# Kernel tuning notes

Hardware: AMD Instinct MI355X
Metric: run time of the kernel (lower is better)

The kernel has to match this reference:

```python
import jax, jax.numpy as jnp
import numpy as np

P = 8
PARENT = {0: -1, 1: 0, 2: 0, 3: 1, 4: 1, 5: 2, 6: 2, 7: 3}

def _topo_order(parent):
    order = [k for k in range(len(parent)) if parent[k] == -1]
    frontier = list(order)
    while frontier:
        cur = frontier.pop(0)
        for k in range(len(parent)):
            if parent[k] == cur:
                order.append(k)
                frontier.append(k)
    return order

ORDER = _topo_order(PARENT)

def so3_exponential_map(log_rot, eps=1e-4):
    # log_rot: [M,3]; pytorch3d-style Rodrigues with clamped squared norm
    nrms = jnp.sum(log_rot * log_rot, axis=-1)
    theta = jnp.sqrt(jnp.clip(nrms, eps))
    fac1 = jnp.sin(theta) / theta
    fac2 = (1.0 - jnp.cos(theta)) / (theta * theta)
    x, y, z = log_rot[:, 0], log_rot[:, 1], log_rot[:, 2]
    zero = jnp.zeros_like(x)
    K = jnp.stack([zero, -z, y, z, zero, -x, -y, x, zero], axis=-1).reshape(-1, 3, 3)
    I = jnp.eye(3, dtype=log_rot.dtype)
    return fac1[:, None, None] * K + fac2[:, None, None] * (K @ K) + I

def _normalize(v, axis=-1, eps=1e-12):
    return v / jnp.maximum(jnp.linalg.norm(v, axis=axis, keepdims=True), eps)

def setup_inputs():
    key = jax.random.key(0)
    ks = jax.random.split(key, 8)
    N, F, K, Pn = 32, 512, 64000, P
    s = 1.0 / np.sqrt(F)  # keep MLP activations sane
    x = jax.random.normal(ks[0], (N, F), jnp.float32)
    W1 = jax.random.normal(ks[1], (F, F), jnp.float32) * s
    b1 = jnp.zeros((F,), jnp.float32)
    W2 = jax.random.normal(ks[2], (F, F), jnp.float32) * s
    b2 = jnp.zeros((F,), jnp.float32)
    W3 = jax.random.normal(ks[3], (F, Pn * 5), jnp.float32) * s
    b3 = jnp.zeros((Pn * 5,), jnp.float32)
    verts = jax.random.normal(ks[4], (K, 3), jnp.float32)
    rot_center = jax.random.normal(ks[5], (Pn, 3), jnp.float32)
    alpha = jax.random.uniform(ks[6], (K, Pn), jnp.float32)
    alpha = alpha / jnp.sum(alpha, axis=-1, keepdims=True)  # LBS-style weights
    axis = jnp.tile(jnp.array([[1.0, 0.0, 0.0]], jnp.float32), (Pn, 1))
    return {"x": x, "W1": W1, "b1": b1, "W2": W2, "b2": b2, "W3": W3, "b3": b3,
            "verts": verts, "rot_center": rot_center, "alpha": alpha, "axis": axis}

def reference(x, W1, b1, W2, b2, W3, b3, verts, rot_center, alpha, axis):
    N = x.shape[0]
    lrelu = lambda h: jax.nn.leaky_relu(h, 0.01)
    h = lrelu(x @ W1 + b1)
    h = lrelu(h @ W2 + b2)
    vec = (h @ W3 + b3).reshape(N, P, 5)  # num_rots+num_trans = 5
    vec_rot = _normalize(vec[..., :3])    # vec[..., 0:num_rots+1]
    angle = jnp.arctan2(vec_rot[..., 1], vec_rot[..., 0])  # [N,P]
    axis_n = _normalize(axis)
    log_rot = angle[..., None] * axis_n[None]  # [N,P,3]
    R = so3_exponential_map(log_rot.reshape(-1, 3)).reshape(N, P, 3, 3)
    # t is forced to zero in the original forward (if True: t = zeros)
    t_part = rot_center[None] - jnp.einsum('npij,pj->npi', R, rot_center)  # [N,P,3]
    Rg = [None] * P
    tg = [None] * P
    for k in ORDER:  # tiny fixed tree (8 nodes), sequential chain composition
        p = PARENT[k]
        if p == -1:
            Rg[k] = R[:, k]
            tg[k] = t_part[:, k]
        else:
            Rg[k] = jnp.einsum('nij,njk->nik', Rg[p], R[:, k])
            tg[k] = jnp.einsum('nij,nj->ni', Rg[p], t_part[:, k]) + tg[p]
    Rg = jnp.stack(Rg, axis=1)  # [N,P,3,3]
    tg = jnp.stack(tg, axis=1)  # [N,P,3]
    # per-part transform applied to every vertex: [N,K,P,3]
    nsv = jnp.einsum('npij,kj->nkpi', Rg, verts) + tg[:, None]
    arti_verts = jnp.einsum('kp,nkpi->nki', alpha, nsv)  # [N,K,3]
    t_net = jnp.zeros((N, P, 3), x.dtype)
    return (arti_verts, t_net)
```

## Files before the change

### kernel.cpp

```cpp
#include <hip/hip_runtime.h>
#include <math.h>

#define FDIM 512
#define NBATCH 32
#define NPART 8
#define KVERT 64000

__global__ __launch_bounds__(256) void layer_k(const float* __restrict__ in,
                                               const float* __restrict__ W,
                                               const float* __restrict__ bias,
                                               float* __restrict__ out) {
  const int jt = blockIdx.x;
  const int n  = blockIdx.y;
  const int jj = threadIdx.x & 63;
  const int fq = threadIdx.x >> 6;
  const int j  = jt * 64 + jj;
  const float* xr = in + n * FDIM + fq * 128;
  const float* wp = W + (fq * 128) * FDIM + j;
  float acc0 = 0.f, acc1 = 0.f;
#pragma unroll
  for (int i = 0; i < 32; ++i) {
    const float4 xv = *(const float4*)(xr + i * 4);
    acc0 += xv.x * wp[0];
    acc1 += xv.y * wp[FDIM];
    acc0 += xv.z * wp[2 * FDIM];
    acc1 += xv.w * wp[3 * FDIM];
    wp += 4 * FDIM;
  }
  __shared__ float red[256];
  red[threadIdx.x] = acc0 + acc1;
  __syncthreads();
  if (threadIdx.x < 64) {
    const int jo = jt * 64 + threadIdx.x;
    float s = red[threadIdx.x] + red[64 + threadIdx.x] + red[128 + threadIdx.x] +
              red[192 + threadIdx.x] + bias[jo];
    out[n * FDIM + jo] = (s > 0.f) ? s : 0.01f * s;
  }
}

__global__ __launch_bounds__(256) void pose_k(const float* __restrict__ h2,
                                              const float* __restrict__ W3,
                                              const float* __restrict__ b3,
                                              const float* __restrict__ rot_center,
                                              float* __restrict__ G,
                                              float* __restrict__ tnet) {
  const int n = blockIdx.x;
  const int t = threadIdx.x;
  const int lane = t & 63;
  const int w = t >> 6;
  float hl[8];
#pragma unroll
  for (int m = 0; m < 8; ++m) hl[m] = h2[n * FDIM + lane + 64 * m];
  __shared__ float vecL[16];
#pragma unroll
  for (int ii = 0; ii < 4; ++ii) {
    const int i = w + ii * 4;
    const int p = i >> 1;
    const int e = i & 1;
    const int col = p * 5 + e;
    float acc = 0.f;
#pragma unroll
    for (int m = 0; m < 8; ++m) acc += hl[m] * W3[(lane + 64 * m) * 40 + col];
#pragma unroll
    for (int off = 32; off > 0; off >>= 1) acc += __shfl_xor(acc, off, 64);
    if (lane == 0) vecL[i] = acc + b3[col];
  }
  __syncthreads();
  __shared__ float M[NPART][6];
  if (t < NPART) {
    const int p = t;
    const float vx = vecL[2 * p];
    const float vy = vecL[2 * p + 1];
    const float a = atan2f(vy, vx);
    const float th = sqrtf(fmaxf(a * a, 1e-4f));
    const float fac1 = sinf(th) / th;
    const float fac2 = (1.f - cosf(th)) / (th * th);
    const float m00 = 1.f - fac2 * a * a;
    const float m01 = -fac1 * a;
    const float m10 = fac1 * a;
    const float m11 = m00;
    const float cy = rot_center[p * 3 + 1];
    const float cz = rot_center[p * 3 + 2];
    M[p][0] = m00;
    M[p][1] = m01;
    M[p][2] = m10;
    M[p][3] = m11;
    M[p][4] = cy - (m00 * cy + m01 * cz);
    M[p][5] = cz - (m10 * cy + m11 * cz);
  }
  __syncthreads();
  if (t == 0) {
    float Gl[NPART][6];
    const int par[NPART] = {-1, 0, 0, 1, 1, 2, 2, 3};
#pragma unroll
    for (int k = 0; k < NPART; ++k) {
      const int p = par[k];
      if (p < 0) {
#pragma unroll
        for (int c = 0; c < 6; ++c) Gl[k][c] = M[k][c];
      } else {
        Gl[k][0] = Gl[p][0] * M[k][0] + Gl[p][1] * M[k][2];
        Gl[k][1] = Gl[p][0] * M[k][1] + Gl[p][1] * M[k][3];
        Gl[k][2] = Gl[p][2] * M[k][0] + Gl[p][3] * M[k][2];
        Gl[k][3] = Gl[p][2] * M[k][1] + Gl[p][3] * M[k][3];
        Gl[k][4] = Gl[p][0] * M[k][4] + Gl[p][1] * M[k][5] + Gl[p][4];
        Gl[k][5] = Gl[p][2] * M[k][4] + Gl[p][3] * M[k][5] + Gl[p][5];
      }
#pragma unroll
      for (int c = 0; c < 6; ++c) G[n * 48 + k * 6 + c] = Gl[k][c];
    }
  }
  if (t < 24) tnet[n * 24 + t] = 0.f;
}

__global__ __launch_bounds__(256) void art_k(const float* __restrict__ G,
                                             const float* __restrict__ verts,
                                             const float* __restrict__ alpha,
                                             float* __restrict__ out) {
  const int n = blockIdx.y;
  const int k0 = (blockIdx.x * 256 + (int)threadIdx.x) * 4;
  if (k0 >= KVERT) return;
  float g[48];
  const float4* G4 = (const float4*)(G + n * 48);
#pragma unroll
  for (int i = 0; i < 12; ++i) ((float4*)g)[i] = G4[i];
  float a[32];
  const float4* A4 = (const float4*)(alpha + (size_t)k0 * 8);
#pragma unroll
  for (int i = 0; i < 8; ++i) ((float4*)a)[i] = A4[i];
  float v[12];
  const float4* V4 = (const float4*)(verts + (size_t)k0 * 3);
#pragma unroll
  for (int i = 0; i < 3; ++i) ((float4*)v)[i] = V4[i];
  float o[12];
#pragma unroll
  for (int q = 0; q < 4; ++q) {
    const float* al = a + q * 8;
    float sA = 0.f, C00 = 0.f, C01 = 0.f, C10 = 0.f, C11 = 0.f, Ty = 0.f, Tz = 0.f;
#pragma unroll
    for (int p = 0; p < NPART; ++p) {
      const float ap = al[p];
      sA += ap;
      C00 += ap * g[p * 6 + 0];
      C01 += ap * g[p * 6 + 1];
      C10 += ap * g[p * 6 + 2];
      C11 += ap * g[p * 6 + 3];
      Ty += ap * g[p * 6 + 4];
      Tz += ap * g[p * 6 + 5];
    }
    const float vy = v[q * 3 + 1], vz = v[q * 3 + 2];
    o[q * 3 + 0] = sA * v[q * 3 + 0];
    o[q * 3 + 1] = C00 * vy + C01 * vz + Ty;
    o[q * 3 + 2] = C10 * vy + C11 * vz + Tz;
  }
  float4* O4 = (float4*)(out + ((size_t)n * KVERT + k0) * 3);
#pragma unroll
  for (int i = 0; i < 3; ++i) O4[i] = ((float4*)o)[i];
}

extern "C" void kernel_launch(void* const* d_in, const int* in_sizes, int n_in,
                              void* d_out, int out_size, void* d_ws, size_t ws_size,
                              hipStream_t stream) {
  const float* x = (const float*)d_in[0];
  const float* W1 = (const float*)d_in[1];
  const float* b1 = (const float*)d_in[2];
  const float* W2 = (const float*)d_in[3];
  const float* b2 = (const float*)d_in[4];
  const float* W3 = (const float*)d_in[5];
  const float* b3 = (const float*)d_in[6];
  const float* verts = (const float*)d_in[7];
  const float* rot_center = (const float*)d_in[8];
  const float* alpha = (const float*)d_in[9];
  float* out = (float*)d_out;

  float* h1 = (float*)d_ws;
  float* h2 = h1 + NBATCH * FDIM;
  float* G = h2 + NBATCH * FDIM;

  layer_k<<<dim3(8, NBATCH), 256, 0, stream>>>(x, W1, b1, h1);
  layer_k<<<dim3(8, NBATCH), 256, 0, stream>>>(h1, W2, b2, h2);
  pose_k<<<NBATCH, 256, 0, stream>>>(h2, W3, b3, rot_center, G,
                                     out + (size_t)NBATCH * KVERT * 3);
  art_k<<<dim3((KVERT + 1023) / 1024, NBATCH), 256, 0, stream>>>(G, verts, alpha, out);
}
```

Before: 111.9 us.

## Fuse pose head into layer2 and pose chain into articulation kernel

The W3 projection moves into the second MLP layer's epilogue, where each block adds its partial dot products into a zeroed workspace with atomics. The per-batch pose/tree composition is recomputed in every block of the articulation kernel, so the separate pose kernel and its launch go away. The articulation grid shrinks to 16 blocks per batch, each handling 4000 vertices in a loop. The trade-offs are redundant transcendental work per block, atomic contention, and much lower parallelism in the memory-bound vertex pass (512 blocks versus about 2000).

```diff
diff --git a/kernel.cpp b/kernel.cpp
--- a/kernel.cpp
+++ b/kernel.cpp
@@ -6,10 +6,12 @@
 #define NPART 8
 #define KVERT 64000
 
-__global__ __launch_bounds__(256) void layer_k(const float* __restrict__ in,
-                                               const float* __restrict__ W,
-                                               const float* __restrict__ bias,
-                                               float* __restrict__ out) {
+__global__ __launch_bounds__(256) void layer1_k(const float* __restrict__ in,
+                                                const float* __restrict__ W,
+                                                const float* __restrict__ bias,
+                                                float* __restrict__ out,
+                                                float* __restrict__ vecG,
+                                                float* __restrict__ tnet) {
   const int jt = blockIdx.x;
   const int n  = blockIdx.y;
   const int jj = threadIdx.x & 63;
@@ -36,57 +38,81 @@
               red[192 + threadIdx.x] + bias[jo];
     out[n * FDIM + jo] = (s > 0.f) ? s : 0.01f * s;
   }
-}
-
-__global__ __launch_bounds__(256) void pose_k(const float* __restrict__ h2,
-                                              const float* __restrict__ W3,
-                                              const float* __restrict__ b3,
-                                              const float* __restrict__ rot_center,
-                                              float* __restrict__ G,
-                                              float* __restrict__ tnet) {
-  const int n = blockIdx.x;
-  const int t = threadIdx.x;
-  const int lane = t & 63;
-  const int w = t >> 6;
-  float hl[8];
-#pragma unroll
-  for (int m = 0; m < 8; ++m) hl[m] = h2[n * FDIM + lane + 64 * m];
-  __shared__ float vecL[16];
-#pragma unroll
-  for (int ii = 0; ii < 4; ++ii) {
-    const int i = w + ii * 4;
-    const int p = i >> 1;
-    const int e = i & 1;
-    const int col = p * 5 + e;
-    float acc = 0.f;
-#pragma unroll
-    for (int m = 0; m < 8; ++m) acc += hl[m] * W3[(lane + 64 * m) * 40 + col];
-#pragma unroll
-    for (int off = 32; off > 0; off >>= 1) acc += __shfl_xor(acc, off, 64);
-    if (lane == 0) vecL[i] = acc + b3[col];
-  }
-  __syncthreads();
+  if (jt == 0 && threadIdx.x < 16) vecG[n * 16 + threadIdx.x] = 0.f;
+  if (jt == 1 && threadIdx.x < 24) tnet[n * 24 + threadIdx.x] = 0.f;
+}
+
+__global__ __launch_bounds__(256) void layer2_k(const float* __restrict__ in,
+                                                const float* __restrict__ W,
+                                                const float* __restrict__ bias,
+                                                const float* __restrict__ W3,
+                                                float* __restrict__ vecG) {
+  const int jt = blockIdx.x;
+  const int n  = blockIdx.y;
+  const int jj = threadIdx.x & 63;
+  const int fq = threadIdx.x >> 6;
+  const int j  = jt * 64 + jj;
+  const float* xr = in + n * FDIM + fq * 128;
+  const float* wp = W + (fq * 128) * FDIM + j;
+  float acc0 = 0.f, acc1 = 0.f;
+#pragma unroll
+  for (int i = 0; i < 32; ++i) {
+    const float4 xv = *(const float4*)(xr + i * 4);
+    acc0 += xv.x * wp[0];
+    acc1 += xv.y * wp[FDIM];
+    acc0 += xv.z * wp[2 * FDIM];
+    acc1 += xv.w * wp[3 * FDIM];
+    wp += 4 * FDIM;
+  }
+  __shared__ float red[256];
+  red[threadIdx.x] = acc0 + acc1;
+  __syncthreads();
+  if (threadIdx.x < 64) {
+    const int lane = threadIdx.x;
+    const int jrow = jt * 64 + lane;
+    float s = red[lane] + red[64 + lane] + red[128 + lane] + red[192 + lane] +
+              bias[jrow];
+    const float h = (s > 0.f) ? s : 0.01f * s;
+#pragma unroll
+    for (int i = 0; i < 16; ++i) {
+      const int col = (i >> 1) * 5 + (i & 1);
+      float part = h * W3[jrow * 40 + col];
+#pragma unroll
+      for (int off = 32; off > 0; off >>= 1) part += __shfl_xor(part, off, 64);
+      if (lane == 0) atomicAdd(&vecG[n * 16 + i], part);
+    }
+  }
+}
+
+__global__ __launch_bounds__(256) void artpose_k(const float* __restrict__ vecG,
+                                                 const float* __restrict__ b3,
+                                                 const float* __restrict__ rot_center,
+                                                 const float* __restrict__ verts,
+                                                 const float* __restrict__ alpha,
+                                                 float* __restrict__ out) {
+  const int kc = blockIdx.x;
+  const int n  = blockIdx.y;
+  const int t  = threadIdx.x;
   __shared__ float M[NPART][6];
+  __shared__ float Gs[48];
   if (t < NPART) {
     const int p = t;
-    const float vx = vecL[2 * p];
-    const float vy = vecL[2 * p + 1];
+    const float vx = vecG[n * 16 + 2 * p] + b3[p * 5];
+    const float vy = vecG[n * 16 + 2 * p + 1] + b3[p * 5 + 1];
     const float a = atan2f(vy, vx);
     const float th = sqrtf(fmaxf(a * a, 1e-4f));
     const float fac1 = sinf(th) / th;
     const float fac2 = (1.f - cosf(th)) / (th * th);
     const float m00 = 1.f - fac2 * a * a;
     const float m01 = -fac1 * a;
-    const float m10 = fac1 * a;
-    const float m11 = m00;
     const float cy = rot_center[p * 3 + 1];
     const float cz = rot_center[p * 3 + 2];
     M[p][0] = m00;
     M[p][1] = m01;
-    M[p][2] = m10;
-    M[p][3] = m11;
+    M[p][2] = -m01;
+    M[p][3] = m00;
     M[p][4] = cy - (m00 * cy + m01 * cz);
-    M[p][5] = cz - (m10 * cy + m11 * cz);
+    M[p][5] = cz - (-m01 * cy + m00 * cz);
   }
   __syncthreads();
   if (t == 0) {
@@ -107,55 +133,53 @@
         Gl[k][5] = Gl[p][2] * M[k][4] + Gl[p][3] * M[k][5] + Gl[p][5];
       }
 #pragma unroll
-      for (int c = 0; c < 6; ++c) G[n * 48 + k * 6 + c] = Gl[k][c];
+      for (int c = 0; c < 6; ++c) Gs[k * 6 + c] = Gl[k][c];
     }
   }
-  if (t < 24) tnet[n * 24 + t] = 0.f;
-}
-
-__global__ __launch_bounds__(256) void art_k(const float* __restrict__ G,
-                                             const float* __restrict__ verts,
-                                             const float* __restrict__ alpha,
-                                             float* __restrict__ out) {
-  const int n = blockIdx.y;
-  const int k0 = (blockIdx.x * 256 + (int)threadIdx.x) * 4;
-  if (k0 >= KVERT) return;
+  __syncthreads();
   float g[48];
-  const float4* G4 = (const float4*)(G + n * 48);
-#pragma unroll
-  for (int i = 0; i < 12; ++i) ((float4*)g)[i] = G4[i];
-  float a[32];
-  const float4* A4 = (const float4*)(alpha + (size_t)k0 * 8);
-#pragma unroll
-  for (int i = 0; i < 8; ++i) ((float4*)a)[i] = A4[i];
-  float v[12];
-  const float4* V4 = (const float4*)(verts + (size_t)k0 * 3);
-#pragma unroll
-  for (int i = 0; i < 3; ++i) ((float4*)v)[i] = V4[i];
-  float o[12];
-#pragma unroll
-  for (int q = 0; q < 4; ++q) {
-    const float* al = a + q * 8;
-    float sA = 0.f, C00 = 0.f, C01 = 0.f, C10 = 0.f, C11 = 0.f, Ty = 0.f, Tz = 0.f;
-#pragma unroll
-    for (int p = 0; p < NPART; ++p) {
-      const float ap = al[p];
-      sA += ap;
-      C00 += ap * g[p * 6 + 0];
-      C01 += ap * g[p * 6 + 1];
-      C10 += ap * g[p * 6 + 2];
-      C11 += ap * g[p * 6 + 3];
-      Ty += ap * g[p * 6 + 4];
-      Tz += ap * g[p * 6 + 5];
+#pragma unroll
+  for (int i = 0; i < 48; ++i) g[i] = Gs[i];
+#pragma unroll
+  for (int it = 0; it < 4; ++it) {
+    const int qi = it * 256 + t;
+    if (qi < 1000) {
+      const int k0 = kc * 4000 + qi * 4;
+      float a4[32];
+      const float4* A4 = (const float4*)(alpha + (size_t)k0 * 8);
+#pragma unroll
+      for (int i = 0; i < 8; ++i) ((float4*)a4)[i] = A4[i];
+      float v[12];
+      const float4* V4 = (const float4*)(verts + (size_t)k0 * 3);
+#pragma unroll
+      for (int i = 0; i < 3; ++i) ((float4*)v)[i] = V4[i];
+      float o[12];
+#pragma unroll
+      for (int q = 0; q < 4; ++q) {
+        const float* al = a4 + q * 8;
+        float sA = 0.f, C00 = 0.f, C01 = 0.f, C10 = 0.f, C11 = 0.f, Ty = 0.f,
+              Tz = 0.f;
+#pragma unroll
+        for (int p = 0; p < NPART; ++p) {
+          const float ap = al[p];
+          sA += ap;
+          C00 += ap * g[p * 6 + 0];
+          C01 += ap * g[p * 6 + 1];
+          C10 += ap * g[p * 6 + 2];
+          C11 += ap * g[p * 6 + 3];
+          Ty += ap * g[p * 6 + 4];
+          Tz += ap * g[p * 6 + 5];
+        }
+        const float vy = v[q * 3 + 1], vz = v[q * 3 + 2];
+        o[q * 3 + 0] = sA * v[q * 3 + 0];
+        o[q * 3 + 1] = C00 * vy + C01 * vz + Ty;
+        o[q * 3 + 2] = C10 * vy + C11 * vz + Tz;
+      }
+      float4* O4 = (float4*)(out + ((size_t)n * KVERT + k0) * 3);
+#pragma unroll
+      for (int i = 0; i < 3; ++i) O4[i] = ((float4*)o)[i];
     }
-    const float vy = v[q * 3 + 1], vz = v[q * 3 + 2];
-    o[q * 3 + 0] = sA * v[q * 3 + 0];
-    o[q * 3 + 1] = C00 * vy + C01 * vz + Ty;
-    o[q * 3 + 2] = C10 * vy + C11 * vz + Tz;
-  }
-  float4* O4 = (float4*)(out + ((size_t)n * KVERT + k0) * 3);
-#pragma unroll
-  for (int i = 0; i < 3; ++i) O4[i] = ((float4*)o)[i];
+  }
 }
 
 extern "C" void kernel_launch(void* const* d_in, const int* in_sizes, int n_in,
@@ -174,12 +198,11 @@
   float* out = (float*)d_out;
 
   float* h1 = (float*)d_ws;
-  float* h2 = h1 + NBATCH * FDIM;
-  float* G = h2 + NBATCH * FDIM;
-
-  layer_k<<<dim3(8, NBATCH), 256, 0, stream>>>(x, W1, b1, h1);
-  layer_k<<<dim3(8, NBATCH), 256, 0, stream>>>(h1, W2, b2, h2);
-  pose_k<<<NBATCH, 256, 0, stream>>>(h2, W3, b3, rot_center, G,
-                                     out + (size_t)NBATCH * KVERT * 3);
-  art_k<<<dim3((KVERT + 1023) / 1024, NBATCH), 256, 0, stream>>>(G, verts, alpha, out);
-}
+  float* vecG = h1 + NBATCH * FDIM;
+  float* tnet = out + (size_t)NBATCH * KVERT * 3;
+
+  layer1_k<<<dim3(8, NBATCH), 256, 0, stream>>>(x, W1, b1, h1, vecG, tnet);
+  layer2_k<<<dim3(8, NBATCH), 256, 0, stream>>>(h1, W2, b2, W3, vecG);
+  artpose_k<<<dim3(16, NBATCH), 256, 0, stream>>>(vecG, b3, rot_center, verts,
+                                                  alpha, out);
+}
```

Measured after the change: 113.9 us. About the same (+1.9%).
